# Kernel tuning notes

Hardware: AMD Instinct MI355X
Metric: run time of the kernel (lower is better)

## Reference

```python
import jax, jax.numpy as jnp
import numpy as np

B, S, H, L, V = 128, 512, 1024, 4, 32000


def setup_inputs() -> dict:
    key = jax.random.key(0)
    ks = jax.random.split(key, 7)
    lengths = jax.random.randint(ks[0], (B,), 1, S + 1)
    lengths = lengths.at[0].set(S)  # force max length == S so T is static
    tok = jax.random.randint(ks[1], (B, S), 1, V)  # nonzero tokens inside length
    pos = jnp.arange(S)[None, :]
    x = jnp.where(pos < lengths[:, None], tok, 0)  # 0 = pad (x>0 defines length)
    emb = jax.random.normal(ks[2], (V, H), dtype=jnp.float32) * 0.02
    W_ih = jax.random.normal(ks[3], (L, 4 * H, H), dtype=jnp.float32) / np.float32(np.sqrt(H))
    W_hh = jax.random.normal(ks[4], (L, 4 * H, H), dtype=jnp.float32) / np.float32(np.sqrt(H))
    b_ih = jax.random.normal(ks[5], (L, 4 * H), dtype=jnp.float32) * 0.01
    b_hh = jax.random.normal(ks[6], (L, 4 * H), dtype=jnp.float32) * 0.01
    return {"x": x, "emb": emb, "W_ih": W_ih, "W_hh": W_hh, "b_ih": b_ih, "b_hh": b_hh}


def reference(x, emb, W_ih, W_hh, b_ih, b_hh):
    # lengths and pack's descending sort (pack_padded_sequence, enforce_sorted=False)
    lengths = jnp.sum(x > 0, axis=1)                         # [B]
    sorted_idx = jnp.argsort(-lengths, stable=True)          # sorted (desc) order
    unsort_idx = jnp.argsort(sorted_idx)                     # packed.unsorted_indices

    # Source bug: `start` is never advanced, so every iteration runs a ONE-step
    # stacked LSTM (zero init state) on packed.data[0:bs_t] == t=0 embeddings of
    # the bs_t longest sequences. Compute that single step once on all rows.
    xt = emb[x[sorted_idx, 0]]                               # [B, H] sorted order
    h0 = jnp.zeros_like(xt)                                  # zero initial hidden
    hs, cs = [], []
    for l in range(W_ih.shape[0]):
        gates = xt @ W_ih[l].T + b_ih[l] + h0 @ W_hh[l].T + b_hh[l]
        i, f, g, o = jnp.split(gates, 4, axis=-1)            # torch LSTMCell order
        c = jax.nn.sigmoid(i) * jnp.tanh(g)                  # f * c0 = 0
        h = jax.nn.sigmoid(o) * jnp.tanh(c)
        xt = h
        hs.append(h)
        cs.append(c)

    # output[t, b] = top-layer h for original seq b, zeroed where t >= lengths[b]
    T = x.shape[1]                                           # max length == S
    h_top = xt[unsort_idx]                                   # back to original order
    tmask = (jnp.arange(T)[:, None] < lengths[None, :]).astype(h_top.dtype)  # [T,B]
    output = tmask[:, :, None] * h_top[None, :, :]           # [T, B, H]

    # state from the LAST loop iteration: sorted order, rows >= bs_last zero-padded
    bs_last = jnp.sum(lengths >= T)                          # batch size at t = T-1
    smask = (jnp.arange(x.shape[0]) < bs_last).astype(h_top.dtype)[None, :, None]
    state_h = jnp.stack(hs, axis=0) * smask                  # [L, B, H]
    state_c = jnp.stack(cs, axis=0) * smask                  # [L, B, H]
    return output, state_h, state_c
```

## Files before the change

kernel.cpp:

```cpp
#include <hip/hip_runtime.h>

#define Bn 128
#define Sn 512
#define Hn 1024
#define Ln 4

typedef float nfloat4 __attribute__((ext_vector_type(4)));

__device__ __forceinline__ float sigmoidf_(float x) { return 1.0f / (1.0f + __expf(-x)); }

__global__ __launch_bounds__(128) void len_kernel(const int* __restrict__ x, int* __restrict__ lengths) {
  const int b = blockIdx.x, t = threadIdx.x;
  int4 v = ((const int4*)x)[b * 128 + t];
  int c = (v.x > 0) + (v.y > 0) + (v.z > 0) + (v.w > 0);
  for (int off = 32; off > 0; off >>= 1) c += __shfl_down(c, off);
  __shared__ int tmp[2];
  if ((t & 63) == 0) tmp[t >> 6] = c;
  __syncthreads();
  if (t == 0) lengths[b] = tmp[0] + tmp[1];
}

__global__ __launch_bounds__(128) void sort_kernel(const int* __restrict__ x, const int* __restrict__ lengths,
                                                   int* __restrict__ rank, int* __restrict__ tok_sorted,
                                                   int* __restrict__ bs_last) {
  __shared__ int sl[128];
  __shared__ int cnt;
  const int b = threadIdx.x;
  const int len = lengths[b];
  sl[b] = len;
  if (b == 0) cnt = 0;
  __syncthreads();
  int r = 0;
  for (int b2 = 0; b2 < 128; b2++) {
    int l2 = sl[b2];
    r += (l2 > len) || (l2 == len && b2 < b);
  }
  rank[b] = r;
  tok_sorted[r] = x[b * Sn];
  if (len >= Sn) atomicAdd(&cnt, 1);
  __syncthreads();
  if (b == 0) bs_last[0] = cnt;
}

__global__ __launch_bounds__(256) void gemm_kernel(const float* __restrict__ xt,
                                                   const int* __restrict__ tok,
                                                   const float* __restrict__ Wl,
                                                   float* __restrict__ part) {
  __shared__ float xtT[32][132];
  __shared__ float Ws[32][96];
  __shared__ int sTok[128];
  const int t = threadIdx.x;
  const int mtile = blockIdx.x & 31;
  const int kc = blockIdx.x >> 5;
  const int rg = t & 31;
  const int msub = t >> 5;
  const int k0 = kc * 128;
  const int kv4 = (t & 7) * 4;

  if (tok != nullptr) {
    if (t < 128) sTok[t] = tok[t];
    __syncthreads();
  }
  const float* xrow[4];
#pragma unroll
  for (int i = 0; i < 4; i++) {
    const int r = i * 32 + (t >> 3);
    const int row = (tok != nullptr) ? sTok[r] : r;
    xrow[i] = xt + (size_t)row * 1024;
  }

  float acc[3][4][4];
#pragma unroll
  for (int q = 0; q < 3; q++)
#pragma unroll
    for (int mm = 0; mm < 4; mm++)
#pragma unroll
      for (int rr = 0; rr < 4; rr++) acc[q][mm][rr] = 0.0f;

  float4 xreg[4], wreg[3];
  {
#pragma unroll
    for (int i = 0; i < 4; i++) xreg[i] = *(const float4*)&xrow[i][k0 + kv4];
#pragma unroll
    for (int i = 0; i < 3; i++) {
      int jj = i * 32 + (t >> 3);
      int q = jj >> 5, mloc = jj & 31;
      int qoff = (q == 0) ? 0 : ((q == 1) ? 2048 : 3072);
      wreg[i] = *(const float4*)&Wl[(size_t)(qoff + mtile * 32 + mloc) * 1024 + k0 + kv4];
    }
  }

#pragma unroll
  for (int tile = 0; tile < 4; tile++) {
    __syncthreads();
#pragma unroll
    for (int i = 0; i < 4; i++) {
      const int r = i * 32 + (t >> 3);
      xtT[kv4 + 0][r] = xreg[i].x;
      xtT[kv4 + 1][r] = xreg[i].y;
      xtT[kv4 + 2][r] = xreg[i].z;
      xtT[kv4 + 3][r] = xreg[i].w;
    }
#pragma unroll
    for (int i = 0; i < 3; i++) {
      const int jj = i * 32 + (t >> 3);
      Ws[kv4 + 0][jj] = wreg[i].x;
      Ws[kv4 + 1][jj] = wreg[i].y;
      Ws[kv4 + 2][jj] = wreg[i].z;
      Ws[kv4 + 3][jj] = wreg[i].w;
    }
    float4 xnxt[4], wnxt[3];
    if (tile < 3) {
      const int kt = k0 + (tile + 1) * 32;
#pragma unroll
      for (int i = 0; i < 4; i++) xnxt[i] = *(const float4*)&xrow[i][kt + kv4];
#pragma unroll
      for (int i = 0; i < 3; i++) {
        int jj = i * 32 + (t >> 3);
        int q = jj >> 5, mloc = jj & 31;
        int qoff = (q == 0) ? 0 : ((q == 1) ? 2048 : 3072);
        wnxt[i] = *(const float4*)&Wl[(size_t)(qoff + mtile * 32 + mloc) * 1024 + kt + kv4];
      }
    }
    __syncthreads();
#pragma unroll
    for (int kk = 0; kk < 32; kk++) {
      const float4 xv = *(const float4*)&xtT[kk][rg * 4];
      const float4 w0 = *(const float4*)&Ws[kk][msub * 4];
      const float4 w1 = *(const float4*)&Ws[kk][32 + msub * 4];
      const float4 w2 = *(const float4*)&Ws[kk][64 + msub * 4];
      const float xa[4] = {xv.x, xv.y, xv.z, xv.w};
      const float wv[3][4] = {{w0.x, w0.y, w0.z, w0.w},
                              {w1.x, w1.y, w1.z, w1.w},
                              {w2.x, w2.y, w2.z, w2.w}};
#pragma unroll
      for (int q = 0; q < 3; q++)
#pragma unroll
        for (int mm = 0; mm < 4; mm++)
#pragma unroll
          for (int rr = 0; rr < 4; rr++)
            acc[q][mm][rr] = fmaf(wv[q][mm], xa[rr], acc[q][mm][rr]);
    }
    if (tile < 3) {
#pragma unroll
      for (int i = 0; i < 4; i++) xreg[i] = xnxt[i];
#pragma unroll
      for (int i = 0; i < 3; i++) wreg[i] = wnxt[i];
    }
  }

  const int mbase = mtile * 32 + msub * 4;
#pragma unroll
  for (int q = 0; q < 3; q++)
#pragma unroll
    for (int mm = 0; mm < 4; mm++) {
      float4 v = make_float4(acc[q][mm][0], acc[q][mm][1], acc[q][mm][2], acc[q][mm][3]);
      *(float4*)&part[(((size_t)kc * 3 + q) * 1024 + (mbase + mm)) * 128 + rg * 4] = v;
    }
}

__global__ __launch_bounds__(128) void act_kernel(const float* __restrict__ part,
                                                  const float* __restrict__ bih,
                                                  const float* __restrict__ bhh,
                                                  const int* __restrict__ bs_last,
                                                  float* __restrict__ xt_out,
                                                  float* __restrict__ sh,
                                                  float* __restrict__ sc) {
  const int r = threadIdx.x;
  const int m0 = blockIdx.x * 4;
  const int bs = bs_last[0];
  float hv[4], cv[4];
#pragma unroll
  for (int mm = 0; mm < 4; mm++) {
    const int m = m0 + mm;
    float si = 0.f, sg = 0.f, so = 0.f;
#pragma unroll
    for (int kc = 0; kc < 8; kc++) {
      const float* p = part + (((size_t)kc * 3) * 1024 + m) * 128 + r;
      si += p[0];
      sg += p[(size_t)1024 * 128];
      so += p[(size_t)2048 * 128];
    }
    si += bih[m] + bhh[m];
    sg += bih[2048 + m] + bhh[2048 + m];
    so += bih[3072 + m] + bhh[3072 + m];
    const float c = sigmoidf_(si) * tanhf(sg);
    const float h = sigmoidf_(so) * tanhf(c);
    hv[mm] = h;
    cv[mm] = c;
  }
  const float msk = (r < bs) ? 1.0f : 0.0f;
  *(float4*)&xt_out[(size_t)r * 1024 + m0] = make_float4(hv[0], hv[1], hv[2], hv[3]);
  *(float4*)&sh[(size_t)r * 1024 + m0] =
      make_float4(msk * hv[0], msk * hv[1], msk * hv[2], msk * hv[3]);
  *(float4*)&sc[(size_t)r * 1024 + m0] =
      make_float4(msk * cv[0], msk * cv[1], msk * cv[2], msk * cv[3]);
}

__global__ __launch_bounds__(256) void bcast_kernel(const float* __restrict__ hfin,
                                                    const int* __restrict__ lengths,
                                                    const int* __restrict__ rank,
                                                    float* __restrict__ out) {
  const int b = blockIdx.x & 127;
  const int c = blockIdx.x >> 7;
  const int len = lengths[b];
  const int t0 = c * 64;
  nfloat4 v = (nfloat4)0.0f;
  if (t0 < len) v = ((const nfloat4*)hfin)[rank[b] * 256 + threadIdx.x];
  int valid = len - t0;
  valid = valid < 0 ? 0 : (valid > 64 ? 64 : valid);
  nfloat4* p = (nfloat4*)out + ((size_t)t0 * 128 + b) * 256 + threadIdx.x;
  for (int i = 0; i < valid; i++) {
    __builtin_nontemporal_store(v, p);
    p += 32768;
  }
  const nfloat4 z = (nfloat4)0.0f;
  for (int i = valid; i < 64; i++) {
    __builtin_nontemporal_store(z, p);
    p += 32768;
  }
}

extern "C" void kernel_launch(void* const* d_in, const int* in_sizes, int n_in,
                              void* d_out, int out_size, void* d_ws, size_t ws_size,
                              hipStream_t stream) {
  const int* x = (const int*)d_in[0];
  const float* emb = (const float*)d_in[1];
  const float* W_ih = (const float*)d_in[2];
  const float* b_ih = (const float*)d_in[4];
  const float* b_hh = (const float*)d_in[5];

  float* out = (float*)d_out;
  float* sh = out + (size_t)Sn * Bn * Hn;
  float* sc = sh + (size_t)Ln * Bn * Hn;
  float* part = out;

  char* ws = (char*)d_ws;
  int* lengths = (int*)ws;
  int* rank = lengths + 128;
  int* tok_sorted = rank + 128;
  int* bs_last = tok_sorted + 128;
  float* xtA = (float*)(ws + 4096);
  float* xtB = xtA + 128 * 1024;

  len_kernel<<<128, 128, 0, stream>>>(x, lengths);
  sort_kernel<<<1, 128, 0, stream>>>(x, lengths, rank, tok_sorted, bs_last);

  float* bufs[2] = {xtA, xtB};
  const float* xin = emb;
  const int* tokp = tok_sorted;
  for (int l = 0; l < Ln; l++) {
    gemm_kernel<<<256, 256, 0, stream>>>(xin, tokp, W_ih + (size_t)l * 4 * Hn * Hn, part);
    act_kernel<<<256, 128, 0, stream>>>(part, b_ih + l * 4 * Hn, b_hh + l * 4 * Hn, bs_last,
                                        bufs[l & 1], sh + (size_t)l * Bn * Hn,
                                        sc + (size_t)l * Bn * Hn);
    xin = bufs[l & 1];
    tokp = nullptr;
  }
  bcast_kernel<<<1024, 256, 0, stream>>>(xin, lengths, rank, out);
}
```

Before: 494.9 us.

## Overlap padding zero-stores with GEMM via extra wavefront and fuse length/sort kernels

```diff
diff --git a/kernel.cpp b/kernel.cpp
--- a/kernel.cpp
+++ b/kernel.cpp
@@ -9,58 +9,98 @@
 
 __device__ __forceinline__ float sigmoidf_(float x) { return 1.0f / (1.0f + __expf(-x)); }
 
-__global__ __launch_bounds__(128) void len_kernel(const int* __restrict__ x, int* __restrict__ lengths) {
-  const int b = blockIdx.x, t = threadIdx.x;
-  int4 v = ((const int4*)x)[b * 128 + t];
-  int c = (v.x > 0) + (v.y > 0) + (v.z > 0) + (v.w > 0);
-  for (int off = 32; off > 0; off >>= 1) c += __shfl_down(c, off);
-  __shared__ int tmp[2];
-  if ((t & 63) == 0) tmp[t >> 6] = c;
-  __syncthreads();
-  if (t == 0) lengths[b] = tmp[0] + tmp[1];
-}
-
-__global__ __launch_bounds__(128) void sort_kernel(const int* __restrict__ x, const int* __restrict__ lengths,
-                                                   int* __restrict__ rank, int* __restrict__ tok_sorted,
-                                                   int* __restrict__ bs_last) {
+__global__ __launch_bounds__(1024) void lensort_kernel(const int* __restrict__ x,
+                                                       int* __restrict__ lengths,
+                                                       int* __restrict__ rank,
+                                                       int* __restrict__ tok_sorted,
+                                                       int* __restrict__ bs_last) {
+  __shared__ int pc[128][8];
   __shared__ int sl[128];
   __shared__ int cnt;
-  const int b = threadIdx.x;
-  const int len = lengths[b];
-  sl[b] = len;
-  if (b == 0) cnt = 0;
+  const int t = threadIdx.x;
+  const int row = t >> 3, seg = t & 7;
+  int c = 0;
+  const int4* xp = (const int4*)x + row * 128 + seg * 16;
+#pragma unroll
+  for (int i = 0; i < 16; i++) {
+    int4 v = xp[i];
+    c += (v.x > 0) + (v.y > 0) + (v.z > 0) + (v.w > 0);
+  }
+  pc[row][seg] = c;
+  if (t == 0) cnt = 0;
   __syncthreads();
-  int r = 0;
-  for (int b2 = 0; b2 < 128; b2++) {
-    int l2 = sl[b2];
-    r += (l2 > len) || (l2 == len && b2 < b);
-  }
-  rank[b] = r;
-  tok_sorted[r] = x[b * Sn];
-  if (len >= Sn) atomicAdd(&cnt, 1);
+  int len = 0;
+  if (t < 128) {
+#pragma unroll
+    for (int i = 0; i < 8; i++) len += pc[t][i];
+    sl[t] = len;
+    lengths[t] = len;
+  }
   __syncthreads();
-  if (b == 0) bs_last[0] = cnt;
-}
-
-__global__ __launch_bounds__(256) void gemm_kernel(const float* __restrict__ xt,
+  if (t < 128) {
+    int r = 0;
+    for (int b2 = 0; b2 < 128; b2++) {
+      int l2 = sl[b2];
+      r += (l2 > len) || (l2 == len && b2 < t);
+    }
+    rank[t] = r;
+    tok_sorted[r] = x[t * Sn];
+    if (len >= Sn) atomicAdd(&cnt, 1);
+  }
+  __syncthreads();
+  if (t == 0) bs_last[0] = cnt;
+}
+
+__global__ __launch_bounds__(320) void gemm_kernel(const float* __restrict__ xt,
                                                    const int* __restrict__ tok,
                                                    const float* __restrict__ Wl,
-                                                   float* __restrict__ part) {
+                                                   float* __restrict__ part,
+                                                   const int* __restrict__ lengths,
+                                                   float* __restrict__ out,
+                                                   const int layer) {
   __shared__ float xtT[32][132];
   __shared__ float Ws[32][96];
   __shared__ int sTok[128];
   const int t = threadIdx.x;
   const int mtile = blockIdx.x & 31;
   const int kc = blockIdx.x >> 5;
+
+  if (tok != nullptr) {
+    if (t < 128) sTok[t] = tok[t];
+    __syncthreads();
+  }
+
+  if (t >= 256) {
+    const int lane = t - 256;
+    const int b = blockIdx.x & 127;
+    const int half = blockIdx.x >> 7;
+    const int len = lengths[b];
+    const int tw0 = 32 + layer * 120 + half * 60;
+    const nfloat4 z = (nfloat4)0.0f;
+#pragma unroll
+    for (int tile = 0; tile < 4; tile++) {
+      __builtin_amdgcn_s_barrier();
+      const int r0 = tw0 + tile * 15;
+      for (int i = 0; i < 15; i++) {
+        const int tt = r0 + i;
+        if (tt >= len) {
+          nfloat4* p = (nfloat4*)out + ((size_t)tt * 128 + b) * 256 + lane * 4;
+          __builtin_nontemporal_store(z, p + 0);
+          __builtin_nontemporal_store(z, p + 1);
+          __builtin_nontemporal_store(z, p + 2);
+          __builtin_nontemporal_store(z, p + 3);
+        }
+      }
+      __builtin_amdgcn_s_barrier();
+    }
+    return;
+  }
+
   const int rg = t & 31;
   const int msub = t >> 5;
   const int k0 = kc * 128;
   const int kv4 = (t & 7) * 4;
 
-  if (tok != nullptr) {
-    if (t < 128) sTok[t] = tok[t];
-    __syncthreads();
-  }
   const float* xrow[4];
 #pragma unroll
   for (int i = 0; i < 4; i++) {
@@ -205,19 +245,22 @@
   const int c = blockIdx.x >> 7;
   const int len = lengths[b];
   const int t0 = c * 64;
-  nfloat4 v = (nfloat4)0.0f;
-  if (t0 < len) v = ((const nfloat4*)hfin)[rank[b] * 256 + threadIdx.x];
-  int valid = len - t0;
-  valid = valid < 0 ? 0 : (valid > 64 ? 64 : valid);
-  nfloat4* p = (nfloat4*)out + ((size_t)t0 * 128 + b) * 256 + threadIdx.x;
-  for (int i = 0; i < valid; i++) {
-    __builtin_nontemporal_store(v, p);
-    p += 32768;
-  }
-  const nfloat4 z = (nfloat4)0.0f;
-  for (int i = valid; i < 64; i++) {
-    __builtin_nontemporal_store(z, p);
-    p += 32768;
+  if (t0 < len) {
+    const nfloat4 v = ((const nfloat4*)hfin)[rank[b] * 256 + threadIdx.x];
+    const int hi = (len < t0 + 64) ? len : (t0 + 64);
+    nfloat4* p = (nfloat4*)out + ((size_t)t0 * 128 + b) * 256 + threadIdx.x;
+    for (int tt = t0; tt < hi; tt++) {
+      __builtin_nontemporal_store(v, p);
+      p += 32768;
+    }
+  }
+  if (c == 0 && len < 32) {
+    const nfloat4 z = (nfloat4)0.0f;
+    nfloat4* pz = (nfloat4*)out + ((size_t)len * 128 + b) * 256 + threadIdx.x;
+    for (int tt = len; tt < 32; tt++) {
+      __builtin_nontemporal_store(z, pz);
+      pz += 32768;
+    }
   }
 }
 
@@ -243,14 +286,14 @@
   float* xtA = (float*)(ws + 4096);
   float* xtB = xtA + 128 * 1024;
 
-  len_kernel<<<128, 128, 0, stream>>>(x, lengths);
-  sort_kernel<<<1, 128, 0, stream>>>(x, lengths, rank, tok_sorted, bs_last);
+  lensort_kernel<<<1, 1024, 0, stream>>>(x, lengths, rank, tok_sorted, bs_last);
 
   float* bufs[2] = {xtA, xtB};
   const float* xin = emb;
   const int* tokp = tok_sorted;
   for (int l = 0; l < Ln; l++) {
-    gemm_kernel<<<256, 256, 0, stream>>>(xin, tokp, W_ih + (size_t)l * 4 * Hn * Hn, part);
+    gemm_kernel<<<256, 320, 0, stream>>>(xin, tokp, W_ih + (size_t)l * 4 * Hn * Hn, part,
+                                         lengths, out, l);
     act_kernel<<<256, 128, 0, stream>>>(part, b_ih + l * 4 * Hn, b_hh + l * 4 * Hn, bs_last,
                                         bufs[l & 1], sh + (size_t)l * Bn * Hn,
                                         sc + (size_t)l * Bn * Hn);
```

Result: slower. 544.2 us (+10.0%).
